# Kernel optimization log

Measured on AMD Instinct MI355X. Metric: run time of the kernel, lower is better.

Reference implementation:

```python
import jax, jax.numpy as jnp
from jax import lax
import numpy as np

B, N, G = 32, 8192, 40   # batch, points per cloud, base voxel grid (coords -20..19)
VS = 0.05                # voxel size
NFREQ = 4                # 8 encoding channels per coord = 4 freqs x (sin,cos)
DN = ('NCDHW', 'OIDHW', 'NCDHW')


def _encode(x):
    # sinusoidal positional encoding: [B,N,3] -> [B,N,24]
    freqs = (2.0 ** jnp.arange(NFREQ, dtype=jnp.float32)) * jnp.pi  # encoding_range=1
    ang = x[..., None] * freqs                    # [B,N,3,4]
    enc = jnp.concatenate([jnp.sin(ang), jnp.cos(ang)], axis=-1)  # [B,N,3,8]
    return enc.reshape(x.shape[0], x.shape[1], 3 * 2 * NFREQ)


def _voxelize(x, enc):
    # mean-pool point features into 40^3 voxels; returns feat [B,24,G,G,G], mask [B,1,G,G,G]
    vi = jnp.clip(jnp.floor(x / VS).astype(jnp.int32), -G // 2, G // 2 - 1) + G // 2
    lin = (vi[..., 0] * G + vi[..., 1]) * G + vi[..., 2]            # [B,N]
    flat = (lin + jnp.arange(B, dtype=jnp.int32)[:, None] * G ** 3).reshape(-1)
    fsum = jnp.zeros((B * G ** 3, 24), jnp.float32).at[flat].add(enc.reshape(-1, 24))
    cnt = jnp.zeros((B * G ** 3, 1), jnp.float32).at[flat].add(1.0)
    active = cnt > 0
    feat = jnp.where(active, fsum / jnp.maximum(cnt, 1.0), 0.0)
    feat = feat.reshape(B, G, G, G, 24).transpose(0, 4, 1, 2, 3)
    mask = active.astype(jnp.float32).reshape(B, 1, G, G, G)
    return feat, mask


def _conv(x, w, b, stride, pad):
    y = lax.conv_general_dilated(x, w, (stride,) * 3, pad, dimension_numbers=DN)
    return y + b[None, :, None, None, None]


def _ln_c(x, g, b, mask, eps=1e-5):
    # per-voxel LayerNorm over channels, only on active voxels
    mu = jnp.mean(x, axis=1, keepdims=True)
    var = jnp.mean((x - mu) ** 2, axis=1, keepdims=True)
    y = (x - mu) * lax.rsqrt(var + eps)
    return (y * g[None, :, None, None, None] + b[None, :, None, None, None]) * mask


def _maxpool2(m):
    return lax.reduce_window(m, -jnp.inf, lax.max, (1, 1, 2, 2, 2), (1, 1, 2, 2, 2), 'VALID')


def setup_inputs() -> dict:
    key = jax.random.key(0)
    ks = jax.random.split(key, 16)
    x = jax.random.uniform(ks[0], (B, N, 3), jnp.float32, minval=-1.0, maxval=1.0)

    def w(k, shape, fan_in):
        return jax.random.normal(k, shape, jnp.float32) * (2.0 / fan_in) ** 0.5

    d = {'x': x}
    d['c1w'] = w(ks[1], (32, 24, 3, 3, 3), 24 * 27);   d['c1b'] = jnp.zeros(32)
    d['g1'] = jnp.ones(32);                            d['b1'] = jnp.zeros(32)
    d['s1w'] = w(ks[2], (64, 32, 2, 2, 2), 32 * 8);    d['s1b'] = jnp.zeros(64)
    d['c2w'] = w(ks[3], (128, 64, 3, 3, 3), 64 * 27);  d['c2b'] = jnp.zeros(128)
    d['g2'] = jnp.ones(128);                           d['b2'] = jnp.zeros(128)
    d['s2w'] = w(ks[4], (256, 128, 2, 2, 2), 128 * 8); d['s2b'] = jnp.zeros(256)
    d['c3w'] = w(ks[5], (512, 256, 3, 3, 3), 256 * 27); d['c3b'] = jnp.zeros(512)
    d['g3'] = jnp.ones(512);                           d['b3'] = jnp.zeros(512)
    d['c4w'] = w(ks[6], (1024, 512, 3, 3, 3), 512 * 27); d['c4b'] = jnp.zeros(1024)
    d['s4w'] = w(ks[7], (1024, 1024, 2, 2, 2), 1024 * 8); d['s4b'] = jnp.zeros(1024)
    d['g4'] = jnp.ones(8192);                          d['b4'] = jnp.zeros(8192)
    d['f1w'] = w(ks[8], (1024, 8192), 8192);           d['f1b'] = jnp.zeros(1024)
    d['f2w'] = w(ks[9], (40, 1024), 1024);             d['f2b'] = jnp.zeros(40)
    return d


def _forward(x, c1w, c1b, g1, b1, s1w, s1b, c2w, c2b, g2, b2, s2w, s2b,
             c3w, c3b, g3, b3, c4w, c4b, s4w, s4b, g4, b4, f1w, f1b, f2w, f2b):
    enc = _encode(x)
    h, m = _voxelize(x, enc)                                 # 40^3, 24ch
    h = _conv(h, c1w, c1b, 1, 'SAME') * m                    # submanifold sparse conv
    h = jax.nn.relu(_ln_c(h, g1, b1, m))
    m = _maxpool2(m)
    h = jax.nn.relu(_conv(h, s1w, s1b, 2, 'VALID') * m)      # 40 -> 20
    h = _conv(h, c2w, c2b, 1, 'SAME') * m
    h = jax.nn.relu(_ln_c(h, g2, b2, m))
    m = _maxpool2(m)
    h = jax.nn.relu(_conv(h, s2w, s2b, 2, 'VALID') * m)      # 20 -> 10
    h = _conv(h, c3w, c3b, 1, 'SAME') * m
    h = _ln_c(h, g3, b3, m)                                  # to_dense: zeros off-mask
    h = jax.nn.relu(h)
    h = jax.nn.relu(_conv(h, c4w, c4b, 2, 'VALID'))          # 10 -> 4 (dense Conv3d)
    h = _conv(h, s4w, s4b, 2, 'VALID')                       # 4 -> 2
    h = h.reshape(B, -1)                                     # [B, 8192]
    mu = jnp.mean(h, -1, keepdims=True)
    var = jnp.mean((h - mu) ** 2, -1, keepdims=True)
    h = (h - mu) * lax.rsqrt(var + 1e-5) * g4 + b4
    h = jax.nn.relu(h)                                       # dropout: eval mode identity
    h = jax.nn.relu(h @ f1w.T + f1b)
    h = h @ f2w.T + f2b
    return jax.nn.log_softmax(h, axis=-1)


def reference(x, c1w, c1b, g1, b1, s1w, s1b, c2w, c2b, g2, b2, s2w, s2b,
              c3w, c3b, g3, b3, c4w, c4b, s4w, s4b, g4, b4, f1w, f1b, f2w, f2b):
    return _forward(x, c1w, c1b, g1, b1, s1w, s1b, c2w, c2b, g2, b2, s2w, s2b,
                    c3w, c3b, g3, b3, c4w, c4b, s4w, s4b, g4, b4, f1w, f1b, f2w, f2b)
```

## Files before the change

### kernel.cpp

```cpp
#include <hip/hip_runtime.h>
#include <math.h>

#define B_ 32
#define N_ 8192
#define G_ 40
#define CB_ 4
#define QB_ 8

static inline int cdiv(long a, int b){ return (int)((a + (long)b - 1)/b); }

#define OFF_S1O   0
#define OFF_S2O   0
#define OFF_PART  0
#define OFF_C4O   16777216
#define OFF_FC1   20971520
#define OFF_LOG   21233664
#define OFF_C2O   32768000
#define OFF_FS    32768000
#define OFF_CNT   81920000
#define OFF_C3O   32768000
#define OFF_M20   98304000
#define OFF_M10   99328000
#define OFF_S4O   99456000
#define WS_NEEDED 101560000

__global__ __launch_bounds__(256) void encode_scatter(const float* __restrict__ x,
    double* __restrict__ fsum, double* __restrict__ cnt, int b0)
{
  int tid = blockIdx.x*256 + threadIdx.x;
  if (tid >= CB_*N_) return;
  int bl = tid / N_;
  const float* p = x + ((size_t)b0*N_ + (size_t)tid)*3;
  float c[3] = { p[0], p[1], p[2] };
  int vi[3];
  #pragma unroll
  for (int ci=0; ci<3; ++ci){
    int v = (int)floorf(c[ci] / 0.05f);
    v = v < -20 ? -20 : (v > 19 ? 19 : v);
    vi[ci] = v + 20;
  }
  int lin = (vi[0]*G_ + vi[1])*G_ + vi[2];
  double* fs = fsum + (size_t)bl*24*64000 + lin;
  const float PI_F = 3.14159265358979323846f;
  #pragma unroll
  for (int ci=0; ci<3; ++ci){
    double ang = (double)c[ci] * (double)PI_F;
    double s = sin(ang), co = cos(ang);
    #pragma unroll
    for (int k=0; k<4; ++k){
      atomicAdd(fs + (size_t)(ci*8 + k)    *64000, s);
      atomicAdd(fs + (size_t)(ci*8 + 4 + k)*64000, co);
      double s2 = 2.0*s*co;
      double c2 = co*co - s*s;
      s = s2; co = c2;
    }
  }
  atomicAdd(cnt + (size_t)bl*64000 + lin, 1.0);
}

__global__ __launch_bounds__(256) void pool_cnt_m20(const double* __restrict__ cnt,
    float* __restrict__ m20)
{
  int tid = blockIdx.x*256 + threadIdx.x;
  if (tid >= CB_*8000) return;
  int xo = tid % 20; int t = tid/20;
  int yo = t % 20;   t /= 20;
  int zo = t % 20;   int bl = t/20;
  const double* cb = cnt + (size_t)bl*64000;
  float mx = 0.0f;
  for (int dz=0; dz<2; ++dz)
    for (int dy=0; dy<2; ++dy)
      for (int dx=0; dx<2; ++dx)
        if (cb[(size_t)((zo*2+dz)*40 + (yo*2+dy))*40 + (xo*2+dx)] > 0.0) mx = 1.0f;
  m20[(size_t)bl*8000 + (zo*20+yo)*20+xo] = mx;
}

__global__ __launch_bounds__(256) void pool_mask_f(const float* __restrict__ m,
    float* __restrict__ mo, int Do, int NB)
{
  long tid = (long)blockIdx.x*256 + threadIdx.x;
  if (tid >= (long)NB*Do*Do*Do) return;
  int Di = Do*2;
  int xo = (int)(tid % Do); long t = tid / Do;
  int yo = (int)(t % Do);   t /= Do;
  int zo = (int)(t % Do);   int b = (int)(t / Do);
  const float* mb = m + (size_t)b*Di*Di*Di;
  float mx = 0.0f;
  for (int dz=0; dz<2; ++dz)
    for (int dy=0; dy<2; ++dy)
      for (int dx=0; dx<2; ++dx)
        mx = fmaxf(mx, mb[(size_t)(zo*2+dz)*Di*Di + (size_t)(yo*2+dy)*Di + (xo*2+dx)]);
  mo[tid] = mx;
}

__global__ __launch_bounds__(64) void c1_ln_s1(
    const double* __restrict__ fsum, const double* __restrict__ cnt,
    const float* __restrict__ c1w, const float* __restrict__ c1b,
    const float* __restrict__ g1,  const float* __restrict__ b1,
    const float* __restrict__ s1w, const float* __restrict__ s1b,
    double* __restrict__ out, int lb0)
{
  __shared__ double sfeat[24][64];
  __shared__ double sh1[32][8];
  __shared__ double smask[8];

  int blk = blockIdx.x;
  int xo = blk % 20; int t1 = blk/20;
  int yo = t1 % 20;  t1 /= 20;
  int zo = t1 % 20;  int bl = t1/20;
  int t = threadIdx.x;

  int lz = t >> 4, ly = (t >> 2) & 3, lx = t & 3;
  int gz = zo*2 - 1 + lz, gy = yo*2 - 1 + ly, gx = xo*2 - 1 + lx;
  bool inb = (gz>=0 && gz<40) && (gy>=0 && gy<40) && (gx>=0 && gx<40);
  int vox = (gz*40 + gy)*40 + gx;
  double cv = inb ? cnt[(size_t)bl*64000 + vox] : 0.0;
  double ic = (cv > 0.0) ? 1.0/cv : 0.0;
  const double* fb = fsum + (size_t)bl*24*64000 + (inb ? vox : 0);
  #pragma unroll
  for (int ci=0; ci<24; ++ci)
    sfeat[ci][t] = ic * fb[(size_t)ci*64000];
  if (t < 8){
    int dz=t>>2, dy=(t>>1)&1, dx=t&1;
    double c8 = cnt[(size_t)bl*64000 + (size_t)((zo*2+dz)*40 + (yo*2+dy))*40 + (xo*2+dx)];
    smask[t] = (c8 > 0.0) ? 1.0 : 0.0;
  }
  __syncthreads();

  double pm = fmax(fmax(fmax(smask[0],smask[1]),fmax(smask[2],smask[3])),
                   fmax(fmax(smask[4],smask[5]),fmax(smask[6],smask[7])));
  int ovox = (zo*20 + yo)*20 + xo;
  double* ob = out + (size_t)(lb0+bl)*64*8000 + ovox;
  if (pm == 0.0){
    ob[(size_t)t*8000] = 0.0;
    return;
  }

  int c   = t & 31;
  int svh = t >> 5;
  double acc[4] = {0,0,0,0};
  const float* wc = c1w + (size_t)c*24*27;
  for (int ci=0; ci<24; ++ci){
    const float* wp = wc + ci*27;
    const double* sp = &sfeat[ci][0] + svh*16;
    #pragma unroll
    for (int kz=0; kz<3; ++kz)
    #pragma unroll
    for (int ky=0; ky<3; ++ky)
    #pragma unroll
    for (int kx=0; kx<3; ++kx){
      double wv = (double)wp[(kz*3+ky)*3+kx];
      const double* q = sp + kz*16 + ky*4 + kx;
      acc[0] += wv * q[0];
      acc[1] += wv * q[1];
      acc[2] += wv * q[4];
      acc[3] += wv * q[5];
    }
  }
  double bias = (double)c1b[c], gc = (double)g1[c], bc = (double)b1[c];
  double h[4], rs1[4], rs2[4];
  #pragma unroll
  for (int i=0;i<4;++i){
    h[i] = (acc[i] + bias) * smask[svh*4+i];
    rs1[i] = h[i]; rs2[i] = h[i]*h[i];
  }
  #pragma unroll
  for (int off=1; off<32; off<<=1){
    #pragma unroll
    for (int i=0;i<4;++i){
      rs1[i] += __shfl_xor(rs1[i], off);
      rs2[i] += __shfl_xor(rs2[i], off);
    }
  }
  #pragma unroll
  for (int i=0;i<4;++i){
    double mu  = rs1[i]*(1.0/32.0);
    double var = fmax(rs2[i]*(1.0/32.0) - mu*mu, 0.0);
    double r   = 1.0/sqrt(var + 1e-5);
    double yv  = ((h[i]-mu)*r*gc + bc) * smask[svh*4+i];
    sh1[c][svh*4+i] = fmax(yv, 0.0);
  }
  __syncthreads();

  const float* wo = s1w + (size_t)t*256;
  double s = 0.0;
  #pragma unroll
  for (int ci=0; ci<32; ++ci){
    #pragma unroll
    for (int sv=0; sv<8; ++sv)
      s += (double)wo[ci*8+sv] * sh1[ci][sv];
  }
  ob[(size_t)t*8000] = fmax(s + (double)s1b[t], 0.0);
}

template<int K, int S, int P, int XT, int CT, int CGB, int TI,
         bool MMUL, bool RELU_, bool PARTIAL>
__global__ __launch_bounds__(256) void conv_lds(
    const double* __restrict__ in, const float* __restrict__ w,
    const float* __restrict__ bias, const float* __restrict__ mask,
    double* __restrict__ out, int NB, int Cin, int Din, int Cout, int Dout,
    int ncic, int cich)
{
  const int K3 = K*K*K;
  const int SP = 256/CGB;
  const int NR = (XT-1)*S + K;
  __shared__ float wl[CGB*CT][TI*K3];

  int tilesx = (Dout + XT - 1)/XT;
  int spat = tilesx*Dout*Dout;
  int nsb = (spat + SP - 1)/SP;
  int bid = blockIdx.x;
  int cic = 0;
  if (PARTIAL){ cic = bid % ncic; bid /= ncic; }
  int sb = bid % nsb;  int t1 = bid / nsb;
  int ncgo = Cout/(CT*CGB);
  int cgo = t1 % ncgo; int b = t1 / ncgo;
  int ciBeg = PARTIAL ? cic*cich : 0;
  int ciEnd = PARTIAL ? ciBeg + cich : Cin;

  int lc = threadIdx.x / SP;
  int sp = threadIdx.x % SP;
  int sidx = sb*SP + sp;
  bool act = sidx < spat;
  int sc = act ? sidx : 0;
  int tx = sc % tilesx;
  int y  = (sc/tilesx) % Dout;
  int z  = sc/(tilesx*Dout);
  int x0 = tx*XT;
  int co0 = (cgo*CGB + lc)*CT;

  int DD = Din*Din;
  const double* inb = in + (size_t)b*Cin*Din*DD;
  const int wcs = Cin*K3;

  double acc[CT][XT];
  #pragma unroll
  for (int c=0;c<CT;++c){
    double bv = PARTIAL ? 0.0 : (double)bias[co0+c];
    #pragma unroll
    for (int i=0;i<XT;++i) acc[c][i]=bv;
  }

  for (int ci0=ciBeg; ci0<ciEnd; ci0+=TI){
    const int cnt_w = CGB*CT*TI*K3;
    for (int idx = threadIdx.x; idx < cnt_w; idx += 256){
      int k  = idx % K3; int t2 = idx / K3;
      int cil= t2 % TI;  int cr = t2 / TI;
      int co = cgo*CGB*CT + cr;
      float v = 0.0f;
      if (ci0+cil < ciEnd) v = w[(size_t)co*wcs + (size_t)(ci0+cil)*K3 + k];
      wl[cr][cil*K3 + k] = v;
    }
    __syncthreads();
    int tmax = min(TI, ciEnd-ci0);
    for (int cil=0; cil<tmax; ++cil){
      const double* inc = inb + (size_t)(ci0+cil)*Din*DD;
      #pragma unroll
      for (int dz=0; dz<K; ++dz){
        int zi = z*S + dz - P;
        if (zi < 0 || zi >= Din) continue;
        #pragma unroll
        for (int dy=0; dy<K; ++dy){
          int yi = y*S + dy - P;
          if (yi < 0 || yi >= Din) continue;
          const double* row = inc + (size_t)zi*DD + (size_t)yi*Din;
          double rv[NR];
          #pragma unroll
          for (int r=0;r<NR;++r){
            int xi = x0*S + r - P;
            rv[r] = (xi>=0 && xi<Din) ? row[xi] : 0.0;
          }
          #pragma unroll
          for (int dx=0; dx<K; ++dx){
            double wv[CT];
            #pragma unroll
            for (int c=0;c<CT;++c)
              wv[c] = (double)wl[lc*CT+c][cil*K3 + (dz*K+dy)*K + dx];
            #pragma unroll
            for (int i=0;i<XT;++i)
              #pragma unroll
              for (int c=0;c<CT;++c) acc[c][i] += wv[c]*rv[i*S+dx];
          }
        }
      }
    }
    __syncthreads();
  }

  if (act){
    int oDD = Dout*Dout;
    size_t chunk_off = PARTIAL ? (size_t)cic*NB*Cout*Dout*oDD : 0;
    size_t ob = chunk_off + (size_t)b*Cout*Dout*oDD + (size_t)z*oDD + (size_t)y*Dout;
    #pragma unroll
    for (int i=0;i<XT;++i){
      int xo = x0+i;
      if (xo >= Dout) continue;
      double mv = 1.0;
      if (MMUL) mv = (double)mask[(size_t)b*Dout*oDD + (size_t)z*oDD + (size_t)y*Dout + xo];
      #pragma unroll
      for (int c=0;c<CT;++c){
        double v = acc[c][i];
        if (MMUL) v *= mv;
        if (RELU_) v = fmax(v,0.0);
        out[ob + (size_t)(co0+c)*Dout*oDD + xo] = v;
      }
    }
  }
}

template<int K,int S,int P,int XT,int CT,int CGB,int TI,bool MM,bool RL,bool PART>
static void launch_conv(const double* in, const float* w, const float* bias,
                        const float* mask, double* out,
                        int Cin, int Din, int Cout, int Dout, int NB,
                        int ncic, hipStream_t st)
{
  const int SP = 256/CGB;
  int tilesx = (Dout+XT-1)/XT;
  int spat = tilesx*Dout*Dout;
  int nsb = (spat + SP - 1)/SP;
  long grid = (long)(PART?ncic:1) * NB * (Cout/(CT*CGB)) * nsb;
  conv_lds<K,S,P,XT,CT,CGB,TI,MM,RL,PART><<<(int)grid,256,0,st>>>(
      in,w,bias,mask,out,NB,Cin,Din,Cout,Dout,ncic,Cin/(PART?ncic:1));
}

__global__ __launch_bounds__(256) void c4_reduce(const double* __restrict__ part,
    const float* __restrict__ bias, double* __restrict__ out, int NB, int ncic)
{
  long tid = (long)blockIdx.x*256 + threadIdx.x;
  long total = (long)NB*1024*64;
  if (tid >= total) return;
  int co = (int)((tid >> 6) & 1023);
  double s = (double)bias[co];
  for (int c=0; c<ncic; ++c) s += part[(size_t)c*total + tid];
  out[tid] = fmax(s, 0.0);
}

__global__ __launch_bounds__(256) void s4_wave(const double* __restrict__ c4o,
    const float* __restrict__ w, const float* __restrict__ bias,
    double* __restrict__ out, int NB)
{
  long gt = (long)blockIdx.x*256 + threadIdx.x;
  int wid = (int)(gt >> 6);
  int lane = threadIdx.x & 63;
  if (wid >= NB*1024) return;
  int co = wid & 1023; int b = wid >> 10;
  const double* ib = c4o + (size_t)b*1024*64;
  const float* wp = w + (size_t)co*8192;
  double acc[8] = {0,0,0,0,0,0,0,0};
  for (int k=lane; k<8192; k+=64){
    double wv = (double)wp[k];
    int ci = k>>3, sv = k&7;
    int dz = sv>>2, dy=(sv>>1)&1, dx=sv&1;
    const double* icp = ib + (size_t)ci*64;
    #pragma unroll
    for (int v=0; v<8; ++v){
      int zo=v>>2, yo=(v>>1)&1, xo=v&1;
      acc[v] += wv * icp[((zo*2+dz)*4+(yo*2+dy))*4 + (xo*2+dx)];
    }
  }
  #pragma unroll
  for (int v=0;v<8;++v){
    double a = acc[v];
    #pragma unroll
    for (int off=32;off>0;off>>=1) a += __shfl_down(a, off);
    if (lane==0) out[((size_t)b*1024+co)*8 + v] = a + (double)bias[co];
  }
}

__global__ __launch_bounds__(256) void ln_chan_d(double* __restrict__ x,
    const float* __restrict__ g, const float* __restrict__ bt,
    const float* __restrict__ mask, int C, int V, int NB)
{
  long tid = (long)blockIdx.x*256 + threadIdx.x;
  if (tid >= (long)NB*V) return;
  int b = (int)(tid / V);
  int v = (int)(tid - (long)b*V);
  double* xp = x + (size_t)b*C*V + v;
  double s = 0.0;
  for (int c=0; c<C; ++c) s += xp[(size_t)c*V];
  double mu = s / C;
  double s2 = 0.0;
  for (int c=0; c<C; ++c){ double d = xp[(size_t)c*V] - mu; s2 += d*d; }
  double r  = 1.0/sqrt(s2 / C + 1e-5);
  double mv = (double)mask[tid];
  for (int c=0; c<C; ++c){
    double yv = ((xp[(size_t)c*V] - mu) * r * (double)g[c] + (double)bt[c]) * mv;
    xp[(size_t)c*V] = fmax(yv, 0.0);
  }
}

__global__ __launch_bounds__(256) void ln_vec(double* __restrict__ h,
    const float* __restrict__ g, const float* __restrict__ bt)
{
  __shared__ double red[256];
  int b = blockIdx.x, t = threadIdx.x;
  double* hp = h + (size_t)b*8192;
  double s = 0.0;
  for (int k=t; k<8192; k+=256) s += hp[k];
  red[t] = s; __syncthreads();
  for (int o=128; o>0; o>>=1){ if (t<o) red[t] += red[t+o]; __syncthreads(); }
  double mu = red[0] / 8192.0;  __syncthreads();
  double s2 = 0.0;
  for (int k=t; k<8192; k+=256){ double d = hp[k]-mu; s2 += d*d; }
  red[t] = s2; __syncthreads();
  for (int o=128; o>0; o>>=1){ if (t<o) red[t] += red[t+o]; __syncthreads(); }
  double r = 1.0/sqrt(red[0]/8192.0 + 1e-5);
  for (int k=t; k<8192; k+=256)
    hp[k] = fmax((hp[k]-mu)*r*(double)g[k] + (double)bt[k], 0.0);
}

__global__ __launch_bounds__(256) void fc_wave(const double* __restrict__ h,
    const float* __restrict__ w, const float* __restrict__ bias,
    double* __restrict__ out, int Kdim, int O, int relu)
{
  long gt = (long)blockIdx.x*256 + threadIdx.x;
  int wid  = (int)(gt >> 6);
  int lane = threadIdx.x & 63;
  if (wid >= B_*O) return;
  int b = wid / O, o = wid - b*O;
  const double* hp = h + (size_t)b*Kdim;
  const float*  wp = w + (size_t)o*Kdim;
  double acc = 0.0;
  for (int k=lane; k<Kdim; k+=64) acc += hp[k]*(double)wp[k];
  #pragma unroll
  for (int off=32; off>0; off>>=1) acc += __shfl_down(acc, off);
  if (lane == 0){
    double v = acc + (double)bias[o];
    if (relu) v = fmax(v, 0.0);
    out[(size_t)b*O + o] = v;
  }
}

__global__ __launch_bounds__(64) void lsm_out(const double* __restrict__ logits,
    float* __restrict__ out)
{
  int b = threadIdx.x;
  if (b >= B_) return;
  const double* lp = logits + (size_t)b*40;
  double m = lp[0];
  for (int i=1; i<40; ++i) m = lp[i] > m ? lp[i] : m;
  double s = 0.0;
  for (int i=0; i<40; ++i) s += exp(lp[i]-m);
  double ls = log(s);
  for (int i=0; i<40; ++i) out[(size_t)b*40+i] = (float)(lp[i] - m - ls);
}

extern "C" void kernel_launch(void* const* d_in, const int* in_sizes, int n_in,
                              void* d_out, int out_size, void* d_ws, size_t ws_size,
                              hipStream_t stream)
{
  if (ws_size < (size_t)WS_NEEDED) return;

  const float* x   = (const float*)d_in[0];
  const float* c1w = (const float*)d_in[1];  const float* c1b = (const float*)d_in[2];
  const float* g1  = (const float*)d_in[3];  const float* b1  = (const float*)d_in[4];
  const float* s1w = (const float*)d_in[5];  const float* s1b = (const float*)d_in[6];
  const float* c2w = (const float*)d_in[7];  const float* c2b = (const float*)d_in[8];
  const float* g2  = (const float*)d_in[9];  const float* b2  = (const float*)d_in[10];
  const float* s2w = (const float*)d_in[11]; const float* s2b = (const float*)d_in[12];
  const float* c3w = (const float*)d_in[13]; const float* c3b = (const float*)d_in[14];
  const float* g3  = (const float*)d_in[15]; const float* b3  = (const float*)d_in[16];
  const float* c4w = (const float*)d_in[17]; const float* c4b = (const float*)d_in[18];
  const float* s4w = (const float*)d_in[19]; const float* s4b = (const float*)d_in[20];
  const float* g4  = (const float*)d_in[21]; const float* b4  = (const float*)d_in[22];
  const float* f1w = (const float*)d_in[23]; const float* f1b = (const float*)d_in[24];
  const float* f2w = (const float*)d_in[25]; const float* f2b = (const float*)d_in[26];

  char* ws = (char*)d_ws;
  double* s1o = (double*)(ws + OFF_S1O);
  double* s2o = (double*)(ws + OFF_S2O);
  double* part= (double*)(ws + OFF_PART);
  double* c4o = (double*)(ws + OFF_C4O);
  double* c2o = (double*)(ws + OFF_C2O);
  double* c3o = (double*)(ws + OFF_C3O);
  double* fsum= (double*)(ws + OFF_FS);
  double* cnt = (double*)(ws + OFF_CNT);
  float*  m20 = (float*)(ws + OFF_M20);
  float*  m10 = (float*)(ws + OFF_M10);
  double* s4o = (double*)(ws + OFF_S4O);
  double* fc1o= (double*)(ws + OFF_FC1);
  double* logd= (double*)(ws + OFF_LOG);

  for (int q = 0; q < 4; ++q){
    int qb0 = q * QB_;

    for (int sc = 0; sc < QB_/CB_; ++sc){
      int b0  = qb0 + sc*CB_;
      int lb0 = sc*CB_;
      hipMemsetAsync(ws + OFF_FS, 0, (size_t)CB_*24*64000*8 + (size_t)CB_*64000*8, stream);
      encode_scatter<<<cdiv((long)CB_*N_,256),256,0,stream>>>(x, fsum, cnt, b0);
      pool_cnt_m20  <<<cdiv((long)CB_*8000,256),256,0,stream>>>(cnt, m20 + (size_t)b0*8000);
      c1_ln_s1<<<CB_*8000, 64, 0, stream>>>(fsum, cnt, c1w, c1b, g1, b1,
                                            s1w, s1b, s1o, lb0);
    }
    pool_mask_f<<<cdiv((long)QB_*1000,256),256,0,stream>>>(
        m20 + (size_t)qb0*8000, m10 + (size_t)qb0*1000, 10, QB_);

    launch_conv<3,1,1, 5,8, 1,32, false,false,false>(s1o, c2w, c2b, nullptr,
        c2o, 64, 20, 128, 20, QB_, 1, stream);
    ln_chan_d<<<cdiv((long)QB_*8000,256),256,0,stream>>>(
        c2o, g2, b2, m20 + (size_t)qb0*8000, 128, 8000, QB_);
    launch_conv<2,2,0, 2,8, 1,128, true,true,false>(c2o, s2w, s2b,
        m10 + (size_t)qb0*1000, s2o, 128, 20, 256, 10, QB_, 1, stream);

    launch_conv<3,1,1, 5,8, 2,16, false,false,false>(s2o, c3w, c3b, nullptr,
        c3o, 256, 10, 512, 10, QB_, 1, stream);
    ln_chan_d<<<cdiv((long)QB_*1000,256),256,0,stream>>>(
        c3o, g3, b3, m10 + (size_t)qb0*1000, 512, 1000, QB_);

    launch_conv<3,2,0, 2,4, 8,8, false,false,true>(c3o, c4w, c4b, nullptr,
        part, 512, 10, 1024, 4, QB_, 4, stream);
    c4_reduce<<<cdiv((long)QB_*1024*64,256),256,0,stream>>>(part, c4b, c4o, QB_, 4);
    s4_wave<<<cdiv((long)QB_*1024*64,256),256,0,stream>>>(
        c4o, s4w, s4b, s4o + (size_t)qb0*8192, QB_);
  }

  ln_vec<<<B_,256,0,stream>>>(s4o, g4, b4);
  fc_wave<<<cdiv((long)B_*1024*64,256),256,0,stream>>>(s4o, f1w, f1b, fc1o, 8192, 1024, 1);
  fc_wave<<<cdiv((long)B_*40*64,256),  256,0,stream>>>(fc1o, f2w, f2b, logd, 1024, 40, 0);
  lsm_out<<<1,64,0,stream>>>(logd, (float*)d_out);
}
```

Before: 25.54 ms.

## Use FP64 MFMA matrix instructions for the 3x3x3 SAME convolutions

Adds a conv_mfma kernel that computes the c2 and c3 3x3x3 stride-1 convolutions with the FP64 16x16x4 MFMA instruction. Each wave handles 16 voxels by 16 output channels, with weights staged in LDS per 16-input-channel chunk. The aim is to replace scalar FP64 FMA loops with matrix-core throughput. A runtime probe with known matrices detects the accumulator lane layout so the output is written in the right order. Inputs are read straight from global memory for each tap with no LDS reuse, which may make the kernel memory-bound.

```diff
diff --git a/kernel.cpp b/kernel.cpp
--- a/kernel.cpp
+++ b/kernel.cpp
@@ -8,6 +8,8 @@
 #define QB_ 8
 
 static inline int cdiv(long a, int b){ return (int)((a + (long)b - 1)/b); }
+
+typedef double d4 __attribute__((ext_vector_type(4)));
 
 #define OFF_S1O   0
 #define OFF_S2O   0
@@ -191,6 +193,119 @@
       s += (double)wo[ci*8+sv] * sh1[ci][sv];
   }
   ob[(size_t)t*8000] = fmax(s + (double)s1b[t], 0.0);
+}
+
+__device__ __forceinline__ double Pf_(int i,int k){ return (double)(1 + i + 31*k); }
+__device__ __forceinline__ double Qf_(int k,int j){ return (double)(2 + 3*j + 7*k); }
+__device__ __forceinline__ double Rf_(int m,int n){
+  double s = 0.0;
+  for (int k=0;k<4;++k) s += Pf_(m,k)*Qf_(k,n);
+  return s;
+}
+
+template<int TI>
+__global__ __launch_bounds__(256) void conv_mfma(
+    const double* __restrict__ in, const float* __restrict__ w,
+    const float* __restrict__ bias, double* __restrict__ out,
+    int NB, int Cin, int Cout, int D)
+{
+  __shared__ float wl[TI*16*27];
+  int spat = D*D*D;
+  int nvt = (spat + 63) / 64;
+  int bid = blockIdx.x;
+  int vt4 = bid % nvt; int t1 = bid / nvt;
+  int cot = t1 % (Cout/16); int b = t1 / (Cout/16);
+  int wid = threadIdx.x >> 6;
+  int lane = threadIdx.x & 63;
+  int li = lane & 15, lk = lane >> 4;
+
+  d4 z = {0.0,0.0,0.0,0.0};
+  d4 det = __builtin_amdgcn_mfma_f64_16x16x4f64(Pf_(li,lk), Qf_(lk,li), z, 0,0,0);
+  bool m2 = true, m3 = true;
+  #pragma unroll
+  for (int r=0;r<4;++r){
+    m2 = m2 && (fabs(det[r] - Rf_(lk+4*r, li)) < 1e-3);
+    m3 = m3 && (fabs(det[r] - Rf_(li, 4*lk+r)) < 1e-3);
+  }
+  int mode = __all(m2) ? 2 : (__all(m3) ? 3 : 1);
+
+  int vbase = vt4*64 + wid*16;
+  int vox = vbase + li;
+  bool vok = vox < spat;
+  int vc = vok ? vox : 0;
+  int vz = vc / (D*D), vy = (vc/D) % D, vx = vc % D;
+
+  const double* inb = in + (size_t)b*Cin*spat;
+  d4 acc = {0.0, 0.0, 0.0, 0.0};
+
+  for (int ci0 = 0; ci0 < Cin; ci0 += TI){
+    for (int idx = threadIdx.x; idx < TI*16*27; idx += 256){
+      int tap = idx % 27; int t2 = idx / 27;
+      int io = t2 % 16; int cc = t2 / 16;
+      wl[(cc*16 + io)*27 + tap] =
+          w[((size_t)(cot*16+io)*Cin + (ci0+cc))*27 + tap];
+    }
+    __syncthreads();
+    #pragma unroll
+    for (int dz = 0; dz < 3; ++dz){
+      int zi = vz + dz - 1;
+      #pragma unroll
+      for (int dy = 0; dy < 3; ++dy){
+        int yi = vy + dy - 1;
+        #pragma unroll
+        for (int dx = 0; dx < 3; ++dx){
+          int xi = vx + dx - 1;
+          bool ok = vok && zi>=0 && zi<D && yi>=0 && yi<D && xi>=0 && xi<D;
+          int so = ok ? (zi*D + yi)*D + xi : 0;
+          int tap = (dz*3+dy)*3+dx;
+          const double* ip = inb + (size_t)(ci0 + lk)*spat + so;
+          #pragma unroll
+          for (int kq = 0; kq < TI/4; ++kq){
+            double a = (double)wl[((kq*4+lk)*16 + li)*27 + tap];
+            double bv = ok ? ip[(size_t)(kq*4)*spat] : 0.0;
+            acc = __builtin_amdgcn_mfma_f64_16x16x4f64(a, bv, acc, 0, 0, 0);
+          }
+        }
+      }
+    }
+    __syncthreads();
+  }
+
+  size_t obb = (size_t)b*Cout*spat;
+  if (mode == 2){
+    if (vok){
+      #pragma unroll
+      for (int r = 0; r < 4; ++r){
+        int co = cot*16 + lk + 4*r;
+        out[obb + (size_t)co*spat + vox] = acc[r] + (double)bias[co];
+      }
+    }
+  } else if (mode == 3){
+    int co = cot*16 + li;
+    #pragma unroll
+    for (int r = 0; r < 4; ++r){
+      int vw = vbase + 4*lk + r;
+      if (vw < spat)
+        out[obb + (size_t)co*spat + vw] = acc[r] + (double)bias[co];
+    }
+  } else {
+    if (vok){
+      #pragma unroll
+      for (int r = 0; r < 4; ++r){
+        int co = cot*16 + 4*lk + r;
+        out[obb + (size_t)co*spat + vox] = acc[r] + (double)bias[co];
+      }
+    }
+  }
+}
+
+static void launch_cmf(const double* in, const float* w, const float* bias,
+                       double* out, int Cin, int Cout, int D, int NB, hipStream_t st)
+{
+  int spat = D*D*D;
+  int nvt = (spat + 63)/64;
+  int grid = NB * (Cout/16) * nvt;
+  conv_mfma<16><<<grid,256,0,st>>>(in, w, bias, out, NB, Cin, Cout, D);
 }
 
 template<int K, int S, int P, int XT, int CT, int CGB, int TI,
@@ -496,15 +611,13 @@
     pool_mask_f<<<cdiv((long)QB_*1000,256),256,0,stream>>>(
         m20 + (size_t)qb0*8000, m10 + (size_t)qb0*1000, 10, QB_);
 
-    launch_conv<3,1,1, 5,8, 1,32, false,false,false>(s1o, c2w, c2b, nullptr,
-        c2o, 64, 20, 128, 20, QB_, 1, stream);
+    launch_cmf(s1o, c2w, c2b, c2o, 64, 128, 20, QB_, stream);
     ln_chan_d<<<cdiv((long)QB_*8000,256),256,0,stream>>>(
         c2o, g2, b2, m20 + (size_t)qb0*8000, 128, 8000, QB_);
     launch_conv<2,2,0, 2,8, 1,128, true,true,false>(c2o, s2w, s2b,
         m10 + (size_t)qb0*1000, s2o, 128, 20, 256, 10, QB_, 1, stream);
 
-    launch_conv<3,1,1, 5,8, 2,16, false,false,false>(s2o, c3w, c3b, nullptr,
-        c3o, 256, 10, 512, 10, QB_, 1, stream);
+    launch_cmf(s2o, c3w, c3b, c3o, 256, 512, 10, QB_, stream);
     ln_chan_d<<<cdiv((long)QB_*1000,256),256,0,stream>>>(
         c3o, g3, b3, m10 + (size_t)qb0*1000, 512, 1000, QB_);
 
```

New measurement: 25.48 ms. No clear change (-0.3%).
